# Kernel tuning notes

Measured on AMD Instinct MI355X. Metric: run time of the kernel, lower is better.

The kernel has to match this reference:

```python
import jax, jax.numpy as jnp
import numpy as np

B, S, D = 2, 2048, 1024
H, HD = 16, 64


def setup_inputs() -> dict:
    key = jax.random.key(0)
    ks = jax.random.split(key, 6)
    hidden_states = jax.random.normal(ks[0], (B, S, D), dtype=jnp.float32)
    c_attn_w = jax.random.normal(ks[1], (D, 3 * D), dtype=jnp.float32) * 0.02
    c_attn_b = jnp.zeros((3 * D,), dtype=jnp.float32)
    c_proj_w = jax.random.normal(ks[2], (D, D), dtype=jnp.float32) * 0.02
    c_proj_b = jnp.zeros((D,), dtype=jnp.float32)
    basis = jax.random.normal(ks[3], (H, HD, HD), dtype=jnp.float32) * 0.1
    projectors = jnp.einsum('hdr,her->hde', basis, basis)  # basis @ basis.T per head
    return {
        'hidden_states': hidden_states,
        'c_attn_w': c_attn_w,
        'c_attn_b': c_attn_b,
        'c_proj_w': c_proj_w,
        'c_proj_b': c_proj_b,
        'projectors': projectors,
    }


def reference(hidden_states, c_attn_w, c_attn_b, c_proj_w, c_proj_b, projectors):
    # GPT2 Conv1D: out = x @ W + b
    qkv = hidden_states @ c_attn_w + c_attn_b  # [B,S,3D]
    q, k, v = jnp.split(qkv, 3, axis=-1)
    # split heads -> [B,H,S,HD]
    def split_heads(t):
        return t.reshape(B, S, H, HD).transpose(0, 2, 1, 3)
    q, k, v = split_heads(q), split_heads(k), split_heads(v)
    scores = jnp.einsum('bhqd,bhkd->bhqk', q, k) / jnp.sqrt(jnp.float32(HD))
    causal = jnp.tril(jnp.ones((S, S), dtype=bool))
    scores = jnp.where(causal, scores, jnp.finfo(scores.dtype).min)
    probs = jax.nn.softmax(scores, axis=-1)
    attn = jnp.einsum('bhqk,bhkd->bhqd', probs, v)  # [B,H,S,HD]
    # per-head basis projector applied to attention output
    attn = jnp.einsum('bhsd,hde->bhse', attn, projectors)
    # merge heads -> [B,S,D]
    attn = attn.transpose(0, 2, 1, 3).reshape(B, S, D)
    out = attn @ c_proj_w + c_proj_b
    return out
```

## Files before the change

### kernel.cpp

```cpp
#include <hip/hip_runtime.h>

typedef __attribute__((ext_vector_type(8))) short bhalf8;
typedef __attribute__((ext_vector_type(4))) float f32x4;
typedef __attribute__((ext_vector_type(8))) unsigned short u16x8;
typedef __attribute__((ext_vector_type(4))) unsigned short u16x4;

#define BDIM 2
#define SDIM 2048
#define DDIM 1024
#define HDIM 16
#define HDHD 64

#define GLD16(gaddr, laddr)                                                          \
  __builtin_amdgcn_global_load_lds(                                                  \
      (const __attribute__((address_space(1))) unsigned int*)(gaddr),                \
      (__attribute__((address_space(3))) unsigned int*)(laddr), 16, 0, 0)

__device__ __forceinline__ unsigned short f2bf(float f) {
  unsigned u = __builtin_bit_cast(unsigned, f);
  u += 0x7fffu + ((u >> 16) & 1u);
  return (unsigned short)(u >> 16);
}
__device__ __forceinline__ float bf2f(unsigned short u) {
  return __builtin_bit_cast(float, (unsigned)u << 16);
}

__global__ __launch_bounds__(256) void cvt_hidden(const float* __restrict__ x,
                                                  unsigned short* __restrict__ y) {
  size_t i = ((size_t)blockIdx.x * 256 + threadIdx.x) * 4;
  f32x4 v = *(const f32x4*)(x + i);
  u16x4 o;
  o[0] = f2bf(v[0]); o[1] = f2bf(v[1]); o[2] = f2bf(v[2]); o[3] = f2bf(v[3]);
  *(u16x4*)(y + i) = o;
}

__global__ __launch_bounds__(256) void transpose_cvt(const float* __restrict__ W,
                                                     unsigned short* __restrict__ Wt,
                                                     int R, int C) {
  __shared__ float tl[32][33];
  int rt = blockIdx.x * 32, ct = blockIdx.y * 32;
  int r8 = threadIdx.x >> 5, c = threadIdx.x & 31;
#pragma unroll
  for (int i = 0; i < 4; i++)
    tl[r8 + i * 8][c] = W[(size_t)(rt + r8 + i * 8) * C + ct + c];
  __syncthreads();
#pragma unroll
  for (int i = 0; i < 4; i++)
    Wt[(size_t)(ct + r8 + i * 8) * R + rt + c] = f2bf(tl[c][r8 + i * 8]);
}

__global__ __launch_bounds__(256) void make_wproj(const float* __restrict__ proj,
                                                  const float* __restrict__ wproj,
                                                  unsigned short* __restrict__ WT) {
  int h = blockIdx.x, ot = blockIdx.y * 64;
  __shared__ float Pl[64][65];
  __shared__ float Wl[64][65];
  int t = threadIdx.x;
#pragma unroll
  for (int i = 0; i < 16; i++) {
    int idx = t + 256 * i;
    int a = idx >> 6, bc = idx & 63;
    Pl[a][bc] = proj[(size_t)h * 4096 + idx];
    Wl[a][bc] = wproj[(size_t)(h * 64 + a) * 1024 + ot + bc];
  }
  __syncthreads();
  int d = t & 63, ob = t >> 6;
#pragma unroll
  for (int i = 0; i < 16; i++) {
    int o = ob + i * 4;
    float acc = 0.f;
#pragma unroll
    for (int e = 0; e < 64; e++) acc += Pl[d][e] * Wl[e][o];
    WT[(size_t)(ot + o) * 1024 + h * 64 + d] = f2bf(acc);
  }
}

template <int EPI>
__global__ __launch_bounds__(256) void gemm_bt(
    const unsigned short* __restrict__ A, const unsigned short* __restrict__ Bt,
    const float* __restrict__ bias, float* __restrict__ Cf,
    unsigned short* __restrict__ q, unsigned short* __restrict__ k,
    unsigned short* __restrict__ v, int M, int N, int K) {
  __shared__ unsigned short As[128 * 64];
  __shared__ unsigned short Bs[128 * 64];
  const int tid = threadIdx.x;
  const int m0 = blockIdx.y * 128, n0 = blockIdx.x * 128;
  f32x4 acc[4][4];
#pragma unroll
  for (int m = 0; m < 4; m++)
#pragma unroll
    for (int n = 0; n < 4; n++) acc[m][n] = f32x4{0.f, 0.f, 0.f, 0.f};
  const int w = tid >> 6, lane = tid & 63;
  const int wr = (w >> 1) * 64, wc = (w & 1) * 64;
  const int lrow = lane & 15, lg = lane >> 4;

  for (int kt = 0; kt < K; kt += 64) {
    __syncthreads();
#pragma unroll
    for (int i = 0; i < 4; i++) {
      int cl = tid + 256 * i;
      int r = cl >> 3, c = cl & 7;
      int sc = (c ^ (r & 7)) * 8;
      GLD16(A + (size_t)(m0 + r) * K + kt + sc, &As[cl * 8]);
      GLD16(Bt + (size_t)(n0 + r) * K + kt + sc, &Bs[cl * 8]);
    }
    __syncthreads();
#pragma unroll
    for (int kk = 0; kk < 2; kk++) {
      bhalf8 af[4], bfr[4];
#pragma unroll
      for (int m = 0; m < 4; m++) {
        int r = wr + m * 16 + lrow;
        int ch = r * 8 + ((kk * 4 + lg) ^ (r & 7));
        af[m] = *(const bhalf8*)(&As[ch * 8]);
      }
#pragma unroll
      for (int n = 0; n < 4; n++) {
        int r = wc + n * 16 + lrow;
        int ch = r * 8 + ((kk * 4 + lg) ^ (r & 7));
        bfr[n] = *(const bhalf8*)(&Bs[ch * 8]);
      }
#pragma unroll
      for (int m = 0; m < 4; m++)
#pragma unroll
        for (int n = 0; n < 4; n++)
          acc[m][n] = __builtin_amdgcn_mfma_f32_16x16x32_bf16(af[m], bfr[n], acc[m][n], 0, 0, 0);
    }
  }
  const int g = lane >> 4, il = lane & 15;
#pragma unroll
  for (int m = 0; m < 4; m++) {
    int rowb = wr + m * 16 + 4 * g;
#pragma unroll
    for (int n = 0; n < 4; n++) {
      int col = n0 + wc + n * 16 + il;
      float bs = bias[col];
#pragma unroll
      for (int r = 0; r < 4; r++) {
        int row = m0 + rowb + r;
        float val = acc[m][n][r] + bs;
        if (EPI == 0) {
          int which = col >> 10, hh = (col >> 6) & 15, hd = col & 63;
          int b = row >> 11, s = row & 2047;
          size_t idx = ((size_t)(b * 16 + hh) * SDIM + s) * HDHD + hd;
          unsigned short bv = f2bf(which == 0 ? val * 0.1803368801f : val);
          if (which == 0) q[idx] = bv;
          else if (which == 1) k[idx] = bv;
          else v[idx] = bv;
        } else {
          Cf[(size_t)row * N + col] = val;
        }
      }
    }
  }
}

__global__ __launch_bounds__(128, 3) void attn_partial(const unsigned short* __restrict__ Q,
                                                       const unsigned short* __restrict__ Kb,
                                                       const unsigned short* __restrict__ Vb,
                                                       unsigned short* __restrict__ PO,
                                                       float2* __restrict__ ML) {
  __shared__ unsigned short Ks[64][72];
  __shared__ unsigned short Vt[64][72];
  __shared__ unsigned short Ps[2][32][72];
  const int bh = blockIdx.x;
  const int qt = 31 - blockIdx.y;
  const int seg = blockIdx.z;
  const int a = qt >> 3, bq = qt & 7;
  const int nseg = a + 1;
  if (seg >= nseg) return;
  const int k0 = seg * 8;
  const int k1 = min(k0 + 8, qt + 1);

  const int tid = threadIdx.x;
  const int w = tid >> 6, lane = tid & 63;
  const int g = lane >> 4, il = lane & 15;
  const int qbase = qt * 64 + w * 32;
  const size_t bhS = (size_t)bh * SDIM;

  bhalf8 qf[2][2];
#pragma unroll
  for (int f = 0; f < 2; f++) {
    const unsigned short* qp = Q + (bhS + qbase + f * 16 + il) * HDHD + g * 8;
    qf[f][0] = *(const bhalf8*)(qp);
    qf[f][1] = *(const bhalf8*)(qp + 32);
  }
  f32x4 oacc[2][4];
#pragma unroll
  for (int f = 0; f < 2; f++)
#pragma unroll
    for (int i = 0; i < 4; i++) oacc[f][i] = f32x4{0.f, 0.f, 0.f, 0.f};
  float mrun[2] = {-1e30f, -1e30f}, lrun[2] = {0.f, 0.f};

  const int krow = tid >> 1;
  const int kchk = (tid & 1) * 32;
  const int vd0 = (tid & 31) * 2;
  const int vkg = (tid >> 5) * 16;

  u16x8 kr[4];
  unsigned vr[16];
  {
    const size_t kb0 = (bhS + (size_t)k0 * 64) * HDHD;
    const unsigned short* ksrc = Kb + kb0 + krow * HDHD + kchk;
#pragma unroll
    for (int i = 0; i < 4; i++) kr[i] = *(const u16x8*)(ksrc + i * 8);
    const unsigned short* vsrc = Vb + kb0 + (size_t)vkg * HDHD + vd0;
#pragma unroll
    for (int i = 0; i < 16; i++) vr[i] = *(const unsigned*)(vsrc + i * HDHD);
  }

  for (int kt = k0; kt < k1; kt++) {
    __syncthreads();
#pragma unroll
    for (int i = 0; i < 4; i++) *(u16x8*)(&Ks[krow][kchk + i * 8]) = kr[i];
    {
      u16x8 lo0, lo1, hi0, hi1;
#pragma unroll
      for (int i = 0; i < 8; i++) {
        lo0[i] = (unsigned short)(vr[i] & 0xffffu); hi0[i] = (unsigned short)(vr[i] >> 16);
      }
#pragma unroll
      for (int i = 0; i < 8; i++) {
        lo1[i] = (unsigned short)(vr[8 + i] & 0xffffu); hi1[i] = (unsigned short)(vr[8 + i] >> 16);
      }
      *(u16x8*)(&Vt[vd0][vkg]) = lo0;     *(u16x8*)(&Vt[vd0][vkg + 8]) = lo1;
      *(u16x8*)(&Vt[vd0 + 1][vkg]) = hi0; *(u16x8*)(&Vt[vd0 + 1][vkg + 8]) = hi1;
    }
    if (kt + 1 < k1) {
      const size_t kbn = (bhS + (size_t)(kt + 1) * 64) * HDHD;
      const unsigned short* ksrc = Kb + kbn + krow * HDHD + kchk;
#pragma unroll
      for (int i = 0; i < 4; i++) kr[i] = *(const u16x8*)(ksrc + i * 8);
      const unsigned short* vsrc = Vb + kbn + (size_t)vkg * HDHD + vd0;
#pragma unroll
      for (int i = 0; i < 16; i++) vr[i] = *(const unsigned*)(vsrc + i * HDHD);
    }
    __syncthreads();
    f32x4 s[2][4];
#pragma unroll
    for (int f = 0; f < 2; f++)
#pragma unroll
      for (int c = 0; c < 4; c++) s[f][c] = f32x4{0.f, 0.f, 0.f, 0.f};
#pragma unroll
    for (int c = 0; c < 4; c++) {
      bhalf8 kf0 = *(const bhalf8*)(&Ks[c * 16 + il][g * 8]);
      bhalf8 kf1 = *(const bhalf8*)(&Ks[c * 16 + il][32 + g * 8]);
#pragma unroll
      for (int f = 0; f < 2; f++) {
        s[f][c] = __builtin_amdgcn_mfma_f32_16x16x32_bf16(kf0, qf[f][0], s[f][c], 0, 0, 0);
        s[f][c] = __builtin_amdgcn_mfma_f32_16x16x32_bf16(kf1, qf[f][1], s[f][c], 0, 0, 0);
      }
    }
    const bool diag = (kt == qt);
    float lmax[2];
#pragma unroll
    for (int f = 0; f < 2; f++) {
      const int thr = w * 32 + f * 16 + il;
      float lm = -1e30f;
#pragma unroll
      for (int c = 0; c < 4; c++)
#pragma unroll
        for (int r = 0; r < 4; r++) {
          float v = s[f][c][r];
          if (diag && (c * 16 + 4 * g + r > thr)) v = -1e30f;
          s[f][c][r] = v;
          lm = fmaxf(lm, v);
        }
      lm = fmaxf(lm, __shfl_xor(lm, 16));
      lm = fmaxf(lm, __shfl_xor(lm, 32));
      lmax[f] = lm;
    }
    if (!__all((lmax[0] <= mrun[0] + 7.f) && (lmax[1] <= mrun[1] + 7.f))) {
#pragma unroll
      for (int f = 0; f < 2; f++) {
        float mn = fmaxf(mrun[f], lmax[f]);
        float sc = exp2f(mrun[f] - mn);
        mrun[f] = mn;
        lrun[f] *= sc;
#pragma unroll
        for (int df = 0; df < 4; df++)
#pragma unroll
          for (int r = 0; r < 4; r++) oacc[f][df][r] *= sc;
      }
    }
#pragma unroll
    for (int f = 0; f < 2; f++) {
      float rs = 0.f;
#pragma unroll
      for (int c = 0; c < 4; c++) {
        u16x4 pk;
#pragma unroll
        for (int r = 0; r < 4; r++) {
          float pv = exp2f(s[f][c][r] - mrun[f]);
          rs += pv;
          pk[r] = f2bf(pv);
        }
        *(u16x4*)(&Ps[w][f * 16 + il][c * 16 + 4 * g]) = pk;
      }
      rs += __shfl_xor(rs, 16);
      rs += __shfl_xor(rs, 32);
      lrun[f] += rs;
    }
#pragma unroll
    for (int kk = 0; kk < 2; kk++) {
      bhalf8 pf0 = *(const bhalf8*)(&Ps[w][il][kk * 32 + g * 8]);
      bhalf8 pf1 = *(const bhalf8*)(&Ps[w][16 + il][kk * 32 + g * 8]);
#pragma unroll
      for (int df = 0; df < 4; df++) {
        bhalf8 vf = *(const bhalf8*)(&Vt[df * 16 + il][kk * 32 + g * 8]);
        oacc[0][df] = __builtin_amdgcn_mfma_f32_16x16x32_bf16(vf, pf0, oacc[0][df], 0, 0, 0);
        oacc[1][df] = __builtin_amdgcn_mfma_f32_16x16x32_bf16(vf, pf1, oacc[1][df], 0, 0, 0);
      }
    }
  }
  const int pidx = bh * 80 + 4 * a * (a + 1) + bq * (a + 1) + seg;
  __syncthreads();
#pragma unroll
  for (int f = 0; f < 2; f++) {
    float inv = 1.f / lrun[f];
#pragma unroll
    for (int df = 0; df < 4; df++) {
      u16x4 o;
#pragma unroll
      for (int r = 0; r < 4; r++) o[r] = f2bf(oacc[f][df][r] * inv);
      *(u16x4*)(&Ks[w * 32 + f * 16 + il][df * 16 + 4 * g]) = o;
    }
  }
  if (g == 0) {
#pragma unroll
    for (int f = 0; f < 2; f++)
      ML[(size_t)pidx * 64 + w * 32 + f * 16 + il] = make_float2(mrun[f], lrun[f]);
  }
  __syncthreads();
  {
    const int row = tid >> 1, half = (tid & 1) * 32;
    unsigned short* dst = PO + (size_t)pidx * 4096 + (size_t)row * 64 + half;
#pragma unroll
    for (int c8 = 0; c8 < 4; c8++)
      *(u16x8*)(dst + c8 * 8) = *(const u16x8*)(&Ks[row][half + c8 * 8]);
  }
}

__global__ __launch_bounds__(256) void attn_reduce(const unsigned short* __restrict__ PO,
                                                   const float2* __restrict__ ML,
                                                   unsigned short* __restrict__ Om) {
  const int bh = blockIdx.x, qt = blockIdx.y;
  const int a = qt >> 3, bq = qt & 7;
  const int nseg = a + 1;
  const int base = bh * 80 + 4 * a * (a + 1) + bq * (a + 1);
  const int t = threadIdx.x;
  const int r = t >> 2, dc = (t & 3) * 16;
  float2 mls[4];
  float M = -1e30f;
#pragma unroll
  for (int s = 0; s < 4; s++) {
    if (s < nseg) { mls[s] = ML[(size_t)(base + s) * 64 + r]; M = fmaxf(M, mls[s].x); }
  }
  float L = 0.f;
  float O[16];
#pragma unroll
  for (int j = 0; j < 16; j++) O[j] = 0.f;
#pragma unroll
  for (int s = 0; s < 4; s++) {
    if (s < nseg) {
      float wgt = mls[s].y * exp2f(mls[s].x - M);
      L += wgt;
      const unsigned short* p = PO + (size_t)(base + s) * 4096 + r * 64 + dc;
      u16x8 p0 = *(const u16x8*)p, p1 = *(const u16x8*)(p + 8);
#pragma unroll
      for (int j = 0; j < 8; j++) O[j] += wgt * bf2f(p0[j]);
#pragma unroll
      for (int j = 0; j < 8; j++) O[8 + j] += wgt * bf2f(p1[j]);
    }
  }
  float inv = 1.f / L;
  const int b = bh >> 4, h = bh & 15;
  size_t orow = ((size_t)b * SDIM + qt * 64 + r) * DDIM + h * HDHD + dc;
  u16x8 o0, o1;
#pragma unroll
  for (int j = 0; j < 8; j++) o0[j] = f2bf(O[j] * inv);
#pragma unroll
  for (int j = 0; j < 8; j++) o1[j] = f2bf(O[8 + j] * inv);
  *(u16x8*)(Om + orow) = o0;
  *(u16x8*)(Om + orow + 8) = o1;
}

__global__ __launch_bounds__(128, 2) void attn_direct(const unsigned short* __restrict__ Q,
                                                      const unsigned short* __restrict__ Kb,
                                                      const unsigned short* __restrict__ Vb,
                                                      unsigned short* __restrict__ Om) {
  __shared__ unsigned short Ks[64][72];
  __shared__ unsigned short Vt[64][72];
  __shared__ unsigned short Ps[2][32][72];
  const int bh = blockIdx.x;
  const int qt = 31 - blockIdx.y;
  const int tid = threadIdx.x;
  const int w = tid >> 6, lane = tid & 63;
  const int g = lane >> 4, il = lane & 15;
  const int qbase = qt * 64 + w * 32;
  const size_t bhS = (size_t)bh * SDIM;
  bhalf8 qf[2][2];
#pragma unroll
  for (int f = 0; f < 2; f++) {
    const unsigned short* qp = Q + (bhS + qbase + f * 16 + il) * HDHD + g * 8;
    qf[f][0] = *(const bhalf8*)(qp);
    qf[f][1] = *(const bhalf8*)(qp + 32);
  }
  f32x4 oacc[2][4];
#pragma unroll
  for (int f = 0; f < 2; f++)
#pragma unroll
    for (int i = 0; i < 4; i++) oacc[f][i] = f32x4{0.f, 0.f, 0.f, 0.f};
  float mrun[2] = {-1e30f, -1e30f}, lrun[2] = {0.f, 0.f};
  const int krow = tid >> 1, kchk = (tid & 1) * 32;
  const int vd0 = (tid & 31) * 2, vkg = (tid >> 5) * 16;
  const int nt = qt + 1;
  for (int kt = 0; kt < nt; kt++) {
    const size_t kbase = (bhS + (size_t)kt * 64) * HDHD;
    __syncthreads();
    {
      const unsigned short* src = Kb + kbase + krow * HDHD + kchk;
#pragma unroll
      for (int i = 0; i < 4; i++) *(u16x8*)(&Ks[krow][kchk + i * 8]) = *(const u16x8*)(src + i * 8);
    }
    {
      const unsigned short* vsrc = Vb + kbase + (size_t)vkg * HDHD + vd0;
      u16x8 lo0, lo1, hi0, hi1;
#pragma unroll
      for (int i = 0; i < 8; i++) {
        unsigned vv = *(const unsigned*)(vsrc + i * HDHD);
        lo0[i] = (unsigned short)(vv & 0xffffu); hi0[i] = (unsigned short)(vv >> 16);
      }
#pragma unroll
      for (int i = 0; i < 8; i++) {
        unsigned vv = *(const unsigned*)(vsrc + (8 + i) * HDHD);
        lo1[i] = (unsigned short)(vv & 0xffffu); hi1[i] = (unsigned short)(vv >> 16);
      }
      *(u16x8*)(&Vt[vd0][vkg]) = lo0;     *(u16x8*)(&Vt[vd0][vkg + 8]) = lo1;
      *(u16x8*)(&Vt[vd0 + 1][vkg]) = hi0; *(u16x8*)(&Vt[vd0 + 1][vkg + 8]) = hi1;
    }
    __syncthreads();
    f32x4 s[2][4];
#pragma unroll
    for (int f = 0; f < 2; f++)
#pragma unroll
      for (int c = 0; c < 4; c++) s[f][c] = f32x4{0.f, 0.f, 0.f, 0.f};
#pragma unroll
    for (int c = 0; c < 4; c++) {
      bhalf8 kf0 = *(const bhalf8*)(&Ks[c * 16 + il][g * 8]);
      bhalf8 kf1 = *(const bhalf8*)(&Ks[c * 16 + il][32 + g * 8]);
#pragma unroll
      for (int f = 0; f < 2; f++) {
        s[f][c] = __builtin_amdgcn_mfma_f32_16x16x32_bf16(kf0, qf[f][0], s[f][c], 0, 0, 0);
        s[f][c] = __builtin_amdgcn_mfma_f32_16x16x32_bf16(kf1, qf[f][1], s[f][c], 0, 0, 0);
      }
    }
    const bool diag = (kt == qt);
#pragma unroll
    for (int f = 0; f < 2; f++) {
      const int thr = w * 32 + f * 16 + il;
      float p[4][4];
      float lmax = -1e30f;
#pragma unroll
      for (int c = 0; c < 4; c++)
#pragma unroll
        for (int r = 0; r < 4; r++) {
          float v = s[f][c][r];
          if (diag && (c * 16 + 4 * g + r > thr)) v = -1e30f;
          p[c][r] = v;
          lmax = fmaxf(lmax, v);
        }
      lmax = fmaxf(lmax, __shfl_xor(lmax, 16));
      lmax = fmaxf(lmax, __shfl_xor(lmax, 32));
      float mn = fmaxf(mrun[f], lmax);
      float sc = exp2f(mrun[f] - mn);
      mrun[f] = mn;
      float rs = 0.f;
#pragma unroll
      for (int c = 0; c < 4; c++)
#pragma unroll
        for (int r = 0; r < 4; r++) { p[c][r] = exp2f(p[c][r] - mn); rs += p[c][r]; }
      rs += __shfl_xor(rs, 16);
      rs += __shfl_xor(rs, 32);
      lrun[f] = lrun[f] * sc + rs;
#pragma unroll
      for (int df = 0; df < 4; df++)
#pragma unroll
        for (int r = 0; r < 4; r++) oacc[f][df][r] *= sc;
#pragma unroll
      for (int c = 0; c < 4; c++) {
        u16x4 pk;
#pragma unroll
        for (int r = 0; r < 4; r++) pk[r] = f2bf(p[c][r]);
        *(u16x4*)(&Ps[w][f * 16 + il][c * 16 + 4 * g]) = pk;
      }
    }
#pragma unroll
    for (int kk = 0; kk < 2; kk++) {
      bhalf8 pf0 = *(const bhalf8*)(&Ps[w][il][kk * 32 + g * 8]);
      bhalf8 pf1 = *(const bhalf8*)(&Ps[w][16 + il][kk * 32 + g * 8]);
#pragma unroll
      for (int df = 0; df < 4; df++) {
        bhalf8 vf = *(const bhalf8*)(&Vt[df * 16 + il][kk * 32 + g * 8]);
        oacc[0][df] = __builtin_amdgcn_mfma_f32_16x16x32_bf16(vf, pf0, oacc[0][df], 0, 0, 0);
        oacc[1][df] = __builtin_amdgcn_mfma_f32_16x16x32_bf16(vf, pf1, oacc[1][df], 0, 0, 0);
      }
    }
  }
  __syncthreads();
#pragma unroll
  for (int f = 0; f < 2; f++) {
    float inv = 1.f / lrun[f];
#pragma unroll
    for (int df = 0; df < 4; df++) {
      u16x4 o;
#pragma unroll
      for (int r = 0; r < 4; r++) o[r] = f2bf(oacc[f][df][r] * inv);
      *(u16x4*)(&Ks[w * 32 + f * 16 + il][df * 16 + 4 * g]) = o;
    }
  }
  __syncthreads();
  {
    const int row = tid >> 1, half = (tid & 1) * 32;
    const int b = bh >> 4, h = bh & 15;
    size_t obase = ((size_t)b * SDIM + qt * 64 + row) * DDIM + h * HDHD + half;
#pragma unroll
    for (int c8 = 0; c8 < 4; c8++)
      *(u16x8*)(Om + obase + c8 * 8) = *(const u16x8*)(&Ks[row][half + c8 * 8]);
  }
}

extern "C" void kernel_launch(void* const* d_in, const int* in_sizes, int n_in,
                              void* d_out, int out_size, void* d_ws, size_t ws_size,
                              hipStream_t stream) {
  const float* hidden = (const float*)d_in[0];
  const float* attn_w = (const float*)d_in[1];
  const float* attn_b = (const float*)d_in[2];
  const float* proj_w = (const float*)d_in[3];
  const float* proj_b = (const float*)d_in[4];
  const float* projectors = (const float*)d_in[5];
  float* out = (float*)d_out;
  char* ws = (char*)d_ws;
  (void)in_sizes; (void)n_in; (void)out_size;

  unsigned short* hseq   = (unsigned short*)(ws);
  unsigned short* wqkvT  = (unsigned short*)(ws + 8388608);
  unsigned short* qb     = (unsigned short*)(ws + 14680064);
  unsigned short* kb     = (unsigned short*)(ws + 23068672);
  unsigned short* vb     = (unsigned short*)(ws + 31457280);
  unsigned short* attnM  = (unsigned short*)(ws + 39845888);
  unsigned short* wprojT = (unsigned short*)(ws + 48234496);
  unsigned short* PO     = (unsigned short*)(ws + 50331648);
  float2*         ML2    = (float2*)(ws + 71303168);
  const size_t ws_needed = 71303168 + 1310720;

  cvt_hidden<<<dim3(4096), dim3(256), 0, stream>>>(hidden, hseq);
  transpose_cvt<<<dim3(32, 96), dim3(256), 0, stream>>>(attn_w, wqkvT, 1024, 3072);
  make_wproj<<<dim3(16, 16), dim3(256), 0, stream>>>(projectors, proj_w, wprojT);
  gemm_bt<0><<<dim3(24, 32), dim3(256), 0, stream>>>(hseq, wqkvT, attn_b, nullptr,
                                                     qb, kb, vb, 4096, 3072, 1024);
  if (ws_size >= ws_needed) {
    attn_partial<<<dim3(32, 32, 4), dim3(128), 0, stream>>>(qb, kb, vb, PO, ML2);
    attn_reduce<<<dim3(32, 32), dim3(256), 0, stream>>>(PO, ML2, attnM);
  } else {
    attn_direct<<<dim3(32, 32), dim3(128), 0, stream>>>(qb, kb, vb, attnM);
  }
  gemm_bt<1><<<dim3(8, 32), dim3(256), 0, stream>>>(attnM, wprojT, proj_b, out,
                                                    nullptr, nullptr, nullptr, 4096, 1024, 1024);
}
```

Baseline: 171.6 us.

## Split output GEMM into smaller-tile kernel, rebalance attention segments, use hardware bf16 convert

After: 193.0 us. 1.12x slower.

```diff
diff --git a/kernel.cpp b/kernel.cpp
--- a/kernel.cpp
+++ b/kernel.cpp
@@ -1,4 +1,5 @@
 #include <hip/hip_runtime.h>
+#include <hip/hip_bf16.h>
 
 typedef __attribute__((ext_vector_type(8))) short bhalf8;
 typedef __attribute__((ext_vector_type(4))) float f32x4;
@@ -20,6 +21,9 @@
   unsigned u = __builtin_bit_cast(unsigned, f);
   u += 0x7fffu + ((u >> 16) & 1u);
   return (unsigned short)(u >> 16);
+}
+__device__ __forceinline__ unsigned short f2bfc(float f) {
+  return __builtin_bit_cast(unsigned short, __float2bfloat16(f));
 }
 __device__ __forceinline__ float bf2f(unsigned short u) {
   return __builtin_bit_cast(float, (unsigned)u << 16);
@@ -75,10 +79,9 @@
   }
 }
 
-template <int EPI>
-__global__ __launch_bounds__(256) void gemm_bt(
+__global__ __launch_bounds__(256) void gemm_qkv(
     const unsigned short* __restrict__ A, const unsigned short* __restrict__ Bt,
-    const float* __restrict__ bias, float* __restrict__ Cf,
+    const float* __restrict__ bias,
     unsigned short* __restrict__ q, unsigned short* __restrict__ k,
     unsigned short* __restrict__ v, int M, int N, int K) {
   __shared__ unsigned short As[128 * 64];
@@ -139,18 +142,74 @@
       for (int r = 0; r < 4; r++) {
         int row = m0 + rowb + r;
         float val = acc[m][n][r] + bs;
-        if (EPI == 0) {
-          int which = col >> 10, hh = (col >> 6) & 15, hd = col & 63;
-          int b = row >> 11, s = row & 2047;
-          size_t idx = ((size_t)(b * 16 + hh) * SDIM + s) * HDHD + hd;
-          unsigned short bv = f2bf(which == 0 ? val * 0.1803368801f : val);
-          if (which == 0) q[idx] = bv;
-          else if (which == 1) k[idx] = bv;
-          else v[idx] = bv;
-        } else {
-          Cf[(size_t)row * N + col] = val;
-        }
-      }
+        int which = col >> 10, hh = (col >> 6) & 15, hd = col & 63;
+        int b = row >> 11, s = row & 2047;
+        size_t idx = ((size_t)(b * 16 + hh) * SDIM + s) * HDHD + hd;
+        unsigned short bv = f2bf(which == 0 ? val * 0.1803368801f : val);
+        if (which == 0) q[idx] = bv;
+        else if (which == 1) k[idx] = bv;
+        else v[idx] = bv;
+      }
+    }
+  }
+}
+
+__global__ __launch_bounds__(128) void gemm_out(
+    const unsigned short* __restrict__ A, const unsigned short* __restrict__ Bt,
+    const float* __restrict__ bias, float* __restrict__ Cf, int M, int N, int K) {
+  __shared__ unsigned short As[64][72];
+  __shared__ unsigned short Bs[128][72];
+  const int tid = threadIdx.x;
+  const int m0 = blockIdx.y * 64, n0 = blockIdx.x * 128;
+  f32x4 acc[4][4];
+#pragma unroll
+  for (int m = 0; m < 4; m++)
+#pragma unroll
+    for (int n = 0; n < 4; n++) acc[m][n] = f32x4{0.f, 0.f, 0.f, 0.f};
+  const int w = tid >> 6, lane = tid & 63;
+  const int wc = w * 64;
+  const int lrow = lane & 15, lk = (lane >> 4) * 8;
+
+  for (int kt = 0; kt < K; kt += 64) {
+    __syncthreads();
+#pragma unroll
+    for (int i = 0; i < 4; i++) {
+      int cch = tid + 128 * i;
+      int r = cch >> 3, c8 = cch & 7;
+      *(u16x8*)(&As[r][c8 * 8]) = *(const u16x8*)(A + (size_t)(m0 + r) * K + kt + c8 * 8);
+    }
+#pragma unroll
+    for (int i = 0; i < 8; i++) {
+      int cch = tid + 128 * i;
+      int r = cch >> 3, c8 = cch & 7;
+      *(u16x8*)(&Bs[r][c8 * 8]) = *(const u16x8*)(Bt + (size_t)(n0 + r) * K + kt + c8 * 8);
+    }
+    __syncthreads();
+#pragma unroll
+    for (int kk = 0; kk < 2; kk++) {
+      bhalf8 af[4], bfr[4];
+#pragma unroll
+      for (int m = 0; m < 4; m++) af[m] = *(const bhalf8*)(&As[m * 16 + lrow][kk * 32 + lk]);
+#pragma unroll
+      for (int n = 0; n < 4; n++) bfr[n] = *(const bhalf8*)(&Bs[wc + n * 16 + lrow][kk * 32 + lk]);
+#pragma unroll
+      for (int m = 0; m < 4; m++)
+#pragma unroll
+        for (int n = 0; n < 4; n++)
+          acc[m][n] = __builtin_amdgcn_mfma_f32_16x16x32_bf16(af[m], bfr[n], acc[m][n], 0, 0, 0);
+    }
+  }
+  const int g = lane >> 4, il = lane & 15;
+#pragma unroll
+  for (int m = 0; m < 4; m++) {
+    int rowb = m * 16 + 4 * g;
+#pragma unroll
+    for (int n = 0; n < 4; n++) {
+      int col = n0 + wc + n * 16 + il;
+      float bs = bias[col];
+#pragma unroll
+      for (int r = 0; r < 4; r++)
+        Cf[(size_t)(m0 + rowb + r) * N + col] = acc[m][n][r] + bs;
     }
   }
 }
@@ -163,14 +222,16 @@
   __shared__ unsigned short Ks[64][72];
   __shared__ unsigned short Vt[64][72];
   __shared__ unsigned short Ps[2][32][72];
-  const int bh = blockIdx.x;
-  const int qt = 31 - blockIdx.y;
+  const int qt = 31 - blockIdx.x;
+  const int bh = blockIdx.y;
   const int seg = blockIdx.z;
   const int a = qt >> 3, bq = qt & 7;
   const int nseg = a + 1;
   if (seg >= nseg) return;
-  const int k0 = seg * 8;
-  const int k1 = min(k0 + 8, qt + 1);
+  const int n = qt + 1;
+  const int len = (n + nseg - 1) / nseg;
+  const int k0 = seg * len;
+  const int k1 = min(k0 + len, n);
 
   const int tid = threadIdx.x;
   const int w = tid >> 6, lane = tid & 63;
@@ -293,7 +354,7 @@
         for (int r = 0; r < 4; r++) {
           float pv = exp2f(s[f][c][r] - mrun[f]);
           rs += pv;
-          pk[r] = f2bf(pv);
+          pk[r] = f2bfc(pv);
         }
         *(u16x4*)(&Ps[w][f * 16 + il][c * 16 + 4 * g]) = pk;
       }
@@ -322,7 +383,7 @@
     for (int df = 0; df < 4; df++) {
       u16x4 o;
 #pragma unroll
-      for (int r = 0; r < 4; r++) o[r] = f2bf(oacc[f][df][r] * inv);
+      for (int r = 0; r < 4; r++) o[r] = f2bfc(oacc[f][df][r] * inv);
       *(u16x4*)(&Ks[w * 32 + f * 16 + il][df * 16 + 4 * g]) = o;
     }
   }
@@ -378,9 +439,9 @@
   size_t orow = ((size_t)b * SDIM + qt * 64 + r) * DDIM + h * HDHD + dc;
   u16x8 o0, o1;
 #pragma unroll
-  for (int j = 0; j < 8; j++) o0[j] = f2bf(O[j] * inv);
-#pragma unroll
-  for (int j = 0; j < 8; j++) o1[j] = f2bf(O[8 + j] * inv);
+  for (int j = 0; j < 8; j++) o0[j] = f2bfc(O[j] * inv);
+#pragma unroll
+  for (int j = 0; j < 8; j++) o1[j] = f2bfc(O[8 + j] * inv);
   *(u16x8*)(Om + orow) = o0;
   *(u16x8*)(Om + orow + 8) = o1;
 }
@@ -491,7 +552,7 @@
       for (int c = 0; c < 4; c++) {
         u16x4 pk;
 #pragma unroll
-        for (int r = 0; r < 4; r++) pk[r] = f2bf(p[c][r]);
+        for (int r = 0; r < 4; r++) pk[r] = f2bfc(p[c][r]);
         *(u16x4*)(&Ps[w][f * 16 + il][c * 16 + 4 * g]) = pk;
       }
     }
@@ -515,7 +576,7 @@
     for (int df = 0; df < 4; df++) {
       u16x4 o;
 #pragma unroll
-      for (int r = 0; r < 4; r++) o[r] = f2bf(oacc[f][df][r] * inv);
+      for (int r = 0; r < 4; r++) o[r] = f2bfc(oacc[f][df][r] * inv);
       *(u16x4*)(&Ks[w * 32 + f * 16 + il][df * 16 + 4 * g]) = o;
     }
   }
@@ -557,14 +618,14 @@
   cvt_hidden<<<dim3(4096), dim3(256), 0, stream>>>(hidden, hseq);
   transpose_cvt<<<dim3(32, 96), dim3(256), 0, stream>>>(attn_w, wqkvT, 1024, 3072);
   make_wproj<<<dim3(16, 16), dim3(256), 0, stream>>>(projectors, proj_w, wprojT);
-  gemm_bt<0><<<dim3(24, 32), dim3(256), 0, stream>>>(hseq, wqkvT, attn_b, nullptr,
-                                                     qb, kb, vb, 4096, 3072, 1024);
+  gemm_qkv<<<dim3(24, 32), dim3(256), 0, stream>>>(hseq, wqkvT, attn_b,
+                                                   qb, kb, vb, 4096, 3072, 1024);
   if (ws_size >= ws_needed) {
     attn_partial<<<dim3(32, 32, 4), dim3(128), 0, stream>>>(qb, kb, vb, PO, ML2);
     attn_reduce<<<dim3(32, 32), dim3(256), 0, stream>>>(PO, ML2, attnM);
   } else {
     attn_direct<<<dim3(32, 32), dim3(128), 0, stream>>>(qb, kb, vb, attnM);
   }
-  gemm_bt<1><<<dim3(8, 32), dim3(256), 0, stream>>>(attnM, wprojT, proj_b, out,
-                                                    nullptr, nullptr, nullptr, 4096, 1024, 1024);
-}
+  gemm_out<<<dim3(8, 64), dim3(128), 0, stream>>>(attnM, wprojT, proj_b, out,
+                                                  4096, 1024, 1024);
+}
```
